# Optimization experiments

Hardware: AMD Instinct MI355X
Metric: run time of the kernel (lower is better)

The kernel has to match this reference:

```python
import jax, jax.numpy as jnp
import numpy as np

SEQ = 4096
EMBED = 1024


def setup_inputs() -> dict:
    key = jax.random.key(0)
    k1, k2 = jax.random.split(key)
    x = jax.random.normal(k1, (SEQ, EMBED), dtype=jnp.float32)
    # torch Linear(embed, 3*embed): store transposed weight so y = x @ W + b
    W = jax.random.normal(k2, (EMBED, 3 * EMBED), dtype=jnp.float32) * (1.0 / np.sqrt(EMBED))
    b = jnp.zeros((3 * EMBED,), dtype=jnp.float32)
    return {"x": x, "W": W, "b": b}


def reference(x, W, b):
    # QKV projection: [S, 3E] -> chunk along features
    qkv = x @ W + b
    q, k, v = jnp.split(qkv, 3, axis=1)  # each [S, E]
    d = q.shape[-1]
    scale = jnp.sqrt(jnp.asarray(d, dtype=x.dtype))
    logits = (q @ k.T) / scale  # [S, S]
    S = q.shape[0]
    causal = jnp.triu(jnp.ones((S, S), dtype=bool), k=1)
    logits = jnp.where(causal, -jnp.inf, logits)
    w = jax.nn.softmax(logits, axis=1)
    return w @ v  # [S, E]
```

## Files before the change

### kernel.cpp

```cpp
#include <hip/hip_runtime.h>

typedef short s16x8 __attribute__((ext_vector_type(8)));
typedef unsigned short u16;
typedef u16 u16x8 __attribute__((ext_vector_type(8)));
typedef float f32x4 __attribute__((ext_vector_type(4)));

#define SEQ 4096
#define EMBED 1024
#define NQKV 3072

static __device__ __forceinline__ u16 f2bf(float f) {
  unsigned int u = __float_as_uint(f);
  u += 0x7fffu + ((u >> 16) & 1u);
  return (u16)(u >> 16);
}
static __device__ __forceinline__ float bf2f(u16 b) {
  return __uint_as_float(((unsigned int)b) << 16);
}

static __device__ __forceinline__ f32x4 mfma16(s16x8 a, s16x8 b, f32x4 c) {
  return __builtin_amdgcn_mfma_f32_16x16x32_bf16(a, b, c, 0, 0, 0);
}

static __device__ __forceinline__ void gl2lds(const u16* g, u16* l) {
  __builtin_amdgcn_global_load_lds(
      (const __attribute__((address_space(1))) unsigned int*)g,
      (__attribute__((address_space(3))) unsigned int*)l, 16, 0, 0);
}

#define WAITVM(n) asm volatile("s_waitcnt vmcnt(" #n ")" ::: "memory")
#define LGKM0 asm volatile("s_waitcnt lgkmcnt(0)" ::: "memory")
#define BAR() asm volatile("s_waitcnt lgkmcnt(0)\n\ts_barrier" ::: "memory")

__global__ __launch_bounds__(256) void conv_x(const float* __restrict__ x,
                                              u16* __restrict__ xbf) {
  const size_t base = ((size_t)blockIdx.x * 256 + threadIdx.x) * 16;
  u16 tmp[16];
#pragma unroll
  for (int p = 0; p < 4; ++p) {
    float4 v = *reinterpret_cast<const float4*>(&x[base + p * 4]);
    tmp[p * 4 + 0] = f2bf(v.x); tmp[p * 4 + 1] = f2bf(v.y);
    tmp[p * 4 + 2] = f2bf(v.z); tmp[p * 4 + 3] = f2bf(v.w);
  }
  *reinterpret_cast<u16x8*>(&xbf[base]) = *reinterpret_cast<u16x8*>(&tmp[0]);
  *reinterpret_cast<u16x8*>(&xbf[base + 8]) = *reinterpret_cast<u16x8*>(&tmp[8]);
}

__global__ __launch_bounds__(256) void conv_wT(const float* __restrict__ W,
                                               u16* __restrict__ wT) {
  __shared__ u16 t[64][72];
  const int n0 = blockIdx.x * 64;
  const int k0 = blockIdx.y * 64;
  const int tid = threadIdx.x;
  const int rr = tid >> 3, c8 = (tid & 7) * 8;
#pragma unroll
  for (int p = 0; p < 2; ++p) {
    int r = p * 32 + rr;
    float4 a = *reinterpret_cast<const float4*>(&W[(size_t)(k0 + r) * NQKV + n0 + c8]);
    float4 b = *reinterpret_cast<const float4*>(&W[(size_t)(k0 + r) * NQKV + n0 + c8 + 4]);
    t[r][c8 + 0] = f2bf(a.x); t[r][c8 + 1] = f2bf(a.y);
    t[r][c8 + 2] = f2bf(a.z); t[r][c8 + 3] = f2bf(a.w);
    t[r][c8 + 4] = f2bf(b.x); t[r][c8 + 5] = f2bf(b.y);
    t[r][c8 + 6] = f2bf(b.z); t[r][c8 + 7] = f2bf(b.w);
  }
  __syncthreads();
#pragma unroll
  for (int p = 0; p < 2; ++p) {
    int c = p * 32 + rr;
    u16x8 v;
#pragma unroll
    for (int j = 0; j < 8; ++j) v[j] = t[c8 + j][c];
    *reinterpret_cast<u16x8*>(&wT[(size_t)(n0 + c) * EMBED + k0 + c8]) = v;
  }
}


#define GSTAGE32(dst_off, srcbase, stride)                                    \
  {                                                                           \
    _Pragma("unroll") for (int p_ = 0; p_ < 2; ++p_) {                        \
      gl2lds((srcbase) + (size_t)(p_ * 64 + w * 16 + (l >> 2)) * (stride) +   \
                 (l & 3) * 8,                                                 \
             lds_ + (dst_off) + p_ * 2048 + w * 512);                         \
    }                                                                         \
  }

#define MFMA_STEP(aoff, boff)                                                 \
  {                                                                           \
    s16x8 af[4], bfr[4];                                                      \
    _Pragma("unroll") for (int mb = 0; mb < 4; ++mb)                          \
        af[mb] = *reinterpret_cast<const s16x8*>(                             \
            &lds_[(aoff) + (wr + mb * 16 + lr) * 32 + lg * 8]);               \
    _Pragma("unroll") for (int nb = 0; nb < 4; ++nb)                          \
        bfr[nb] = *reinterpret_cast<const s16x8*>(                            \
            &lds_[(boff) + (wc + nb * 16 + lr) * 32 + lg * 8]);               \
    _Pragma("unroll") for (int mb = 0; mb < 4; ++mb)                          \
        _Pragma("unroll") for (int nb = 0; nb < 4; ++nb)                      \
            acc[mb][nb] = mfma16(af[mb], bfr[nb], acc[mb][nb]);               \
  }

#define KLOOP2(n, SRC_A, SA_STRIDE, SRC_B, SB_STRIDE)                         \
  GSTAGE32(0, SRC_A(0), SA_STRIDE);                                           \
  GSTAGE32(8192, SRC_B(0), SB_STRIDE);                                        \
  for (int t = 0; t < (n); ++t) {                                             \
    const int cur_ = t & 1, nx_ = cur_ ^ 1;                                   \
    if (t + 1 < (n)) {                                                        \
      LGKM0;                                                                  \
      GSTAGE32(nx_ * 4096, SRC_A(t + 1), SA_STRIDE);                          \
      GSTAGE32(8192 + nx_ * 4096, SRC_B(t + 1), SB_STRIDE);                   \
      WAITVM(4);                                                              \
    } else {                                                                  \
      WAITVM(0);                                                              \
    }                                                                         \
    BAR();                                                                    \
    MFMA_STEP(cur_ * 4096, 8192 + cur_ * 4096);                               \
    BAR();                                                                    \
  }

__global__ __launch_bounds__(256) void qkv_gemm(const u16* __restrict__ xbf,
                                                const u16* __restrict__ wT,
                                                const float* __restrict__ bias,
                                                u16* __restrict__ qkv,
                                                u16* __restrict__ vT) {
  __shared__ u16 lds_[17408];
  const int b = blockIdx.x;
  const int bs = (b & 7) * 96 + (b >> 3);
  const int bm = bs / 24, bn = bs % 24;
  const int m0 = bm * 128, n0 = bn * 128;
  const int tid = threadIdx.x;
  const int w = tid >> 6, l = tid & 63;
  const int wr = (w >> 1) * 64, wc = (w & 1) * 64;
  const int lg = l >> 4, lr = l & 15;

  f32x4 acc[4][4];
#pragma unroll
  for (int i = 0; i < 4; ++i)
#pragma unroll
    for (int j = 0; j < 4; ++j) acc[i][j] = (f32x4){0.f, 0.f, 0.f, 0.f};

  const u16* xa = xbf + (size_t)m0 * EMBED;
  const u16* wb = wT + (size_t)n0 * EMBED;
#define QA_SRC(t) (xa + (t) * 32)
#define QB_SRC(t) (wb + (t) * 32)
  KLOOP2(32, QA_SRC, EMBED, QB_SRC, EMBED);
#undef QA_SRC
#undef QB_SRC

  if (n0 < 2 * EMBED) {
#pragma unroll
    for (int mb = 0; mb < 4; ++mb)
#pragma unroll
      for (int nb = 0; nb < 4; ++nb) {
        const int col = n0 + wc + nb * 16 + lr;
        const float bv = bias[col];
#pragma unroll
        for (int e = 0; e < 4; ++e) {
          const int row = m0 + wr + mb * 16 + lg * 4 + e;
          qkv[(size_t)row * NQKV + col] = f2bf(acc[mb][nb][e] + bv);
        }
      }
  } else {
    const int vb = n0 - 2 * EMBED;
    __syncthreads();
#pragma unroll
    for (int mb = 0; mb < 4; ++mb)
#pragma unroll
      for (int nb = 0; nb < 4; ++nb) {
        const int cc = wc + nb * 16 + lr;
        const float bv = bias[n0 + cc];
#pragma unroll
        for (int e = 0; e < 4; ++e)
          lds_[(wr + mb * 16 + lg * 4 + e) * 136 + cc] = f2bf(acc[mb][nb][e] + bv);
      }
    __syncthreads();
    const int c = tid >> 1, hf = tid & 1;
#pragma unroll
    for (int j = 0; j < 8; ++j) {
      u16x8 v;
#pragma unroll
      for (int e2 = 0; e2 < 8; ++e2) v[e2] = lds_[(hf * 64 + j * 8 + e2) * 136 + c];
      *reinterpret_cast<u16x8*>(&vT[(size_t)(vb + c) * SEQ + m0 + hf * 64 + j * 8]) = v;
    }
  }
}

__global__ __launch_bounds__(256) void s_gemm(const u16* __restrict__ qkv,
                                              u16* __restrict__ Sp) {
  __shared__ u16 lds_[16384];
  const int b = blockIdx.x;
  const int bs = (b & 7) * 66 + (b >> 3);
  int mt = 0, cum = 0;
  while (cum + mt + 1 <= bs) { cum += mt + 1; ++mt; }
  const int nt = bs - cum;
  const int m0 = mt * 128, n0 = nt * 128;
  const int tid = threadIdx.x;
  const int w = tid >> 6, l = tid & 63;
  const int wr = (w >> 1) * 64, wc = (w & 1) * 64;
  const int lg = l >> 4, lr = l & 15;

  f32x4 acc[4][4];
#pragma unroll
  for (int i = 0; i < 4; ++i)
#pragma unroll
    for (int j = 0; j < 4; ++j) acc[i][j] = (f32x4){0.f, 0.f, 0.f, 0.f};

  const u16* qa = qkv + (size_t)m0 * NQKV;
  const u16* kb = qkv + (size_t)n0 * NQKV + EMBED;
#define SA_SRC(t) (qa + (t) * 32)
#define SB_SRC(t) (kb + (t) * 32)
  KLOOP2(32, SA_SRC, NQKV, SB_SRC, NQKV);
#undef SA_SRC
#undef SB_SRC

  u16* base = Sp + (size_t)bs * 16384;
#pragma unroll
  for (int mb = 0; mb < 4; ++mb)
#pragma unroll
    for (int nb = 0; nb < 4; ++nb) {
      const int cn = wc + nb * 16 + lr;
#pragma unroll
      for (int e = 0; e < 4; ++e) {
        const int rm = wr + mb * 16 + lg * 4 + e;
        base[rm * 128 + cn] = f2bf(acc[mb][nb][e] * 0.03125f);
      }
    }
}

__global__ __launch_bounds__(256) void softmax_rows(u16* __restrict__ Sp) {
  __shared__ float red[8];
  const int bid = blockIdx.x;
  const int tid = threadIdx.x;
  const int w = tid >> 6, l = tid & 63;
  const float NEG = -3.0e38f;

  for (int half = 0; half < 2; ++half) {
    const int r = half ? (4095 - bid) : bid;
    const int mt = r >> 7, rr = r & 127;
    const int Lp = (mt + 1) << 7;
    const size_t tri = (size_t)mt * (mt + 1) / 2;

    float v[16];
    float mx = NEG;
#pragma unroll
    for (int s = 0; s < 2; ++s) {
      const int j = tid * 8 + s * 2048;
      if (j < Lp) {
        const u16* p = Sp + (tri + (j >> 7)) * 16384 + rr * 128 + (j & 127);
        u16x8 xv = *reinterpret_cast<const u16x8*>(p);
#pragma unroll
        for (int e = 0; e < 8; ++e) {
          float f = (j + e <= r) ? bf2f(xv[e]) : NEG;
          v[s * 8 + e] = f;
          mx = fmaxf(mx, f);
        }
      } else {
#pragma unroll
        for (int e = 0; e < 8; ++e) v[s * 8 + e] = NEG;
      }
    }
#pragma unroll
    for (int off = 32; off >= 1; off >>= 1) mx = fmaxf(mx, __shfl_xor(mx, off, 64));
    if (l == 0) red[w] = mx;
    __syncthreads();
    mx = fmaxf(fmaxf(red[0], red[1]), fmaxf(red[2], red[3]));

    float sum = 0.f;
#pragma unroll
    for (int i = 0; i < 16; ++i) {
      float e = __expf(v[i] - mx);
      v[i] = e;
      sum += e;
    }
#pragma unroll
    for (int off = 32; off >= 1; off >>= 1) sum += __shfl_xor(sum, off, 64);
    if (l == 0) red[4 + w] = sum;
    __syncthreads();
    sum = red[4] + red[5] + red[6] + red[7];
    const float inv = 1.f / sum;

#pragma unroll
    for (int s = 0; s < 2; ++s) {
      const int j = tid * 8 + s * 2048;
      if (j < Lp) {
        u16x8 pk;
#pragma unroll
        for (int e = 0; e < 8; ++e) pk[e] = f2bf(v[s * 8 + e] * inv);
        *reinterpret_cast<u16x8*>(Sp + (tri + (j >> 7)) * 16384 + rr * 128 + (j & 127)) = pk;
      }
    }
    __syncthreads();
  }
}

__global__ __launch_bounds__(256) void pv_gemm(const u16* __restrict__ Sp,
                                               const u16* __restrict__ vT,
                                               float* __restrict__ out) {
  __shared__ u16 lds_[16384];
  const int nt = blockIdx.y;
  int s81 = blockIdx.x;
  int mt = 0, cum = 0, ls = 0;
  for (;;) {
    const int ns = (mt + 8) >> 3;
    if (s81 < cum + ns) { ls = s81 - cum; break; }
    cum += ns; ++mt;
  }
  const int m0 = mt * 128, n0 = nt * 128;
  const int k0 = ls * 1024;
  const int kext = (mt + 1) * 128;
  const int kend = (k0 + 1024 < kext) ? (k0 + 1024) : kext;
  const int ksteps = (kend - k0) >> 5;
  const size_t tri = (size_t)mt * (mt + 1) / 2;

  const int tid = threadIdx.x;
  const int w = tid >> 6, l = tid & 63;
  const int wr = (w >> 1) * 64, wc = (w & 1) * 64;
  const int lg = l >> 4, lr = l & 15;

  f32x4 acc[4][4];
#pragma unroll
  for (int i = 0; i < 4; ++i)
#pragma unroll
    for (int j = 0; j < 4; ++j) acc[i][j] = (f32x4){0.f, 0.f, 0.f, 0.f};

#define PA_SRC(t) (Sp + (tri + ((k0 + (t)*32) >> 7)) * 16384 + ((k0 + (t)*32) & 127))
#define PB_SRC(t) (vT + (size_t)n0 * SEQ + k0 + (t)*32)
  KLOOP2(ksteps, PA_SRC, 128, PB_SRC, SEQ);
#undef PA_SRC
#undef PB_SRC

#pragma unroll
  for (int mb = 0; mb < 4; ++mb)
#pragma unroll
    for (int nb = 0; nb < 4; ++nb) {
      const int col = n0 + wc + nb * 16 + lr;
#pragma unroll
      for (int e = 0; e < 4; ++e) {
        const int row = m0 + wr + mb * 16 + lg * 4 + e;
        unsafeAtomicAdd(&out[(size_t)row * EMBED + col], acc[mb][nb][e]);
      }
    }
}

__global__ __launch_bounds__(512) void attn_fb(const u16* __restrict__ qkv,
                                               const u16* __restrict__ vT,
                                               float* __restrict__ out) {
  __shared__ u16 q_lds[16][1032];
  __shared__ u16 kv_lds[8][3][2048];
  __shared__ u16 p_lds[16][136];
  __shared__ float redmax[8][16];
  __shared__ float redsum[8][16];
  const int bid = blockIdx.x;
  const int tid = threadIdx.x;
  const int w = tid >> 6, l = tid & 63;
  const int lg = l >> 4, lr = l & 15;

  const int sr = l >> 4;
  const int scb = (l & 15) * 16;
  const int scolA = ((scb ^ (sr << 4)) >> 1);
  const int scolB = ((scb ^ ((4 + sr) << 4)) >> 1);
  int boff[4];
#pragma unroll
  for (int kk = 0; kk < 4; ++kk)
    boff[kk] = lr * 256 + ((kk * 64 + lg * 16) ^ ((lr & 7) << 4));

  u16* kvb[3] = {&kv_lds[w][0][0], &kv_lds[w][1][0], &kv_lds[w][2][0]};

#define STAGE_K(dc, bufp)                                                     \
  {                                                                           \
    LGKM0;                                                                    \
    const u16* g0 = qkv + (size_t)(kb + w * 16 + sr) * NQKV + EMBED + (dc) * 128; \
    gl2lds(g0 + scolA, (bufp));                                               \
    gl2lds(g0 + 4 * NQKV + scolB, (bufp) + 512);                              \
    gl2lds(g0 + 8 * NQKV + scolA, (bufp) + 1024);                             \
    gl2lds(g0 + 12 * NQKV + scolB, (bufp) + 1536);                            \
  }
#define STAGE_V(j, bufp)                                                      \
  {                                                                           \
    LGKM0;                                                                    \
    const u16* g0 = vT + (size_t)((j) * 128 + w * 16 + sr) * SEQ + kb;        \
    gl2lds(g0 + scolA, (bufp));                                               \
    gl2lds(g0 + 4 * SEQ + scolB, (bufp) + 512);                               \
    gl2lds(g0 + 8 * SEQ + scolA, (bufp) + 1024);                              \
    gl2lds(g0 + 12 * SEQ + scolB, (bufp) + 1536);                             \
  }

  const int qb = bid * 16;
  __syncthreads();
#pragma unroll
  for (int p = 0; p < 4; ++p) {
    int idx = p * 512 + tid;
    int r = idx >> 7, c = (idx & 127) * 8;
    *reinterpret_cast<u16x8*>(&q_lds[r][c]) =
        *reinterpret_cast<const u16x8*>(&qkv[(size_t)(qb + r) * NQKV + c]);
  }
  __syncthreads();
  s16x8 qf[32];
#pragma unroll
  for (int kk = 0; kk < 32; ++kk)
    qf[kk] = *reinterpret_cast<const s16x8*>(&q_lds[lr][kk * 32 + lg * 8]);

  f32x4 o_acc[8];
#pragma unroll
  for (int j = 0; j < 8; ++j) o_acc[j] = (f32x4){0.f, 0.f, 0.f, 0.f};
  float m_st[4], l_st[4];
#pragma unroll
  for (int e = 0; e < 4; ++e) { m_st[e] = -__builtin_inff(); l_st[e] = 0.f; }

  const int n_it = (qb >> 7) + 1;
  for (int it = 0; it < n_it; ++it) {
    const int kb = it << 7;
    const int kcol = kb + w * 16 + lr;

    f32x4 s = (f32x4){0.f, 0.f, 0.f, 0.f};
    STAGE_K(0, kvb[0]);
    STAGE_K(1, kvb[1]);
#pragma unroll
    for (int dc = 0; dc < 8; ++dc) {
      if (dc < 6) {
        STAGE_K(dc + 2, kvb[(dc + 2) % 3]);
      } else if (dc == 6) {
        STAGE_V(0, kvb[2]);
      } else {
        STAGE_V(1, kvb[0]);
      }
      WAITVM(8);
      u16* cur = kvb[dc % 3];
#pragma unroll
      for (int kk = 0; kk < 4; ++kk) {
        s16x8 bfr = *reinterpret_cast<const s16x8*>((const char*)cur + boff[kk]);
        s = mfma16(qf[dc * 4 + kk], bfr, s);
      }
    }

    float sv[4], mx[4];
#pragma unroll
    for (int e = 0; e < 4; ++e) {
      float v = s[e] * 0.03125f;
      sv[e] = (kcol > qb + lg * 4 + e) ? -__builtin_inff() : v;
      mx[e] = sv[e];
    }
#pragma unroll
    for (int off = 1; off < 16; off <<= 1)
#pragma unroll
      for (int e = 0; e < 4; ++e) mx[e] = fmaxf(mx[e], __shfl_xor(mx[e], off, 64));
    if (lr == 0) {
#pragma unroll
      for (int e = 0; e < 4; ++e) redmax[w][lg * 4 + e] = mx[e];
    }
    BAR();

    float m_new[4], sc[4], pv[4], rs[4];
#pragma unroll
    for (int e = 0; e < 4; ++e) {
      float m = m_st[e];
#pragma unroll
      for (int ww = 0; ww < 8; ++ww) m = fmaxf(m, redmax[ww][lg * 4 + e]);
      m_new[e] = m;
      sc[e] = __expf(m_st[e] - m);
      pv[e] = __expf(sv[e] - m);
      rs[e] = pv[e];
    }
#pragma unroll
    for (int off = 1; off < 16; off <<= 1)
#pragma unroll
      for (int e = 0; e < 4; ++e) rs[e] += __shfl_xor(rs[e], off, 64);
    if (lr == 0) {
#pragma unroll
      for (int e = 0; e < 4; ++e) redsum[w][lg * 4 + e] = rs[e];
    }
#pragma unroll
    for (int e = 0; e < 4; ++e) p_lds[lg * 4 + e][w * 16 + lr] = f2bf(pv[e]);
    BAR();

#pragma unroll
    for (int e = 0; e < 4; ++e) {
      float a2 = l_st[e] * sc[e];
#pragma unroll
      for (int ww = 0; ww < 8; ++ww) a2 += redsum[ww][lg * 4 + e];
      l_st[e] = a2;
      m_st[e] = m_new[e];
    }
#pragma unroll
    for (int j = 0; j < 8; ++j)
#pragma unroll
      for (int e = 0; e < 4; ++e) o_acc[j][e] *= sc[e];

    s16x8 pa[4];
#pragma unroll
    for (int kk = 0; kk < 4; ++kk)
      pa[kk] = *reinterpret_cast<const s16x8*>(&p_lds[lr][kk * 32 + lg * 8]);

#pragma unroll
    for (int j = 0; j < 8; ++j) {
      if (j < 6) {
        STAGE_V(j + 2, kvb[(j + 4) % 3]);
        WAITVM(8);
      } else if (j == 6) {
        WAITVM(4);
      } else {
        WAITVM(0);
      }
      u16* cur = kvb[(j + 2) % 3];
#pragma unroll
      for (int kk = 0; kk < 4; ++kk) {
        s16x8 bfr = *reinterpret_cast<const s16x8*>((const char*)cur + boff[kk]);
        o_acc[j] = mfma16(pa[kk], bfr, o_acc[j]);
      }
    }
  }

#pragma unroll
  for (int j = 0; j < 8; ++j) {
    const int col = j * 128 + w * 16 + lr;
#pragma unroll
    for (int e = 0; e < 4; ++e)
      out[(size_t)(qb + lg * 4 + e) * EMBED + col] = o_acc[j][e] / l_st[e];
  }
#undef STAGE_K
#undef STAGE_V
}

extern "C" void kernel_launch(void* const* d_in, const int* in_sizes, int n_in,
                              void* d_out, int out_size, void* d_ws, size_t ws_size,
                              hipStream_t stream) {
  (void)in_sizes; (void)n_in; (void)out_size;
  const float* x = (const float*)d_in[0];
  const float* W = (const float*)d_in[1];
  const float* bias = (const float*)d_in[2];
  float* out = (float*)d_out;

  u16* qkv = (u16*)d_ws;
  u16* vT = qkv + (size_t)SEQ * NQKV;
  u16* wT = (u16*)d_out;
  u16* Sp = (u16*)((char*)d_ws + (32u << 20));

  const size_t need = (32u << 20) + (size_t)528 * 16384 * 2;
  const bool big = ws_size >= need;
  u16* xbf = big ? Sp : (u16*)((char*)d_out + (8u << 20));

  conv_x<<<(SEQ * EMBED) / (256 * 16), 256, 0, stream>>>(x, xbf);
  conv_wT<<<dim3(NQKV / 64, EMBED / 64), 256, 0, stream>>>(W, wT);
  qkv_gemm<<<(SEQ / 128) * (NQKV / 128), 256, 0, stream>>>(xbf, wT, bias, qkv, vT);

  if (big) {
    s_gemm<<<528, 256, 0, stream>>>(qkv, Sp);
    softmax_rows<<<2048, 256, 0, stream>>>(Sp);
    hipMemsetAsync(d_out, 0, (size_t)SEQ * EMBED * sizeof(float), stream);
    pv_gemm<<<dim3(80, 8), 256, 0, stream>>>(Sp, vT, out);
  } else {
    attn_fb<<<SEQ / 16, 512, 0, stream>>>(qkv, vT, out);
  }
}
```

Baseline: 150.1 us.

## Enlarge GEMM tiles to 256x128 across qkv, score and PV kernels

Each workgroup now computes a 256x128 output tile, with 8x4 MFMA accumulators per wave, instead of 128x128. This applies to all three GEMM kernels and is meant to raise operand reuse and cut global/LDS traffic per flop. The causal triangle tiling is remapped so that S blocks skip upper tiles at store time. PV uses a zeroed scratch buffer for the out-of-triangle half of the A tile. In exchange it uses more registers and LDS, launches fewer blocks, wastes some compute on masked tiles, and adds a memset.

```diff
diff --git a/kernel.cpp b/kernel.cpp
--- a/kernel.cpp
+++ b/kernel.cpp
@@ -75,7 +75,7 @@
 }
 
 
-#define GSTAGE32(dst_off, srcbase, stride)                                    \
+#define GST2(dst_off, srcbase, stride)                                        \
   {                                                                           \
     _Pragma("unroll") for (int p_ = 0; p_ < 2; ++p_) {                        \
       gl2lds((srcbase) + (size_t)(p_ * 64 + w * 16 + (l >> 2)) * (stride) +   \
@@ -84,145 +84,160 @@
     }                                                                         \
   }
 
-#define MFMA_STEP(aoff, boff)                                                 \
+#define MFMA256(aoff, boff)                                                   \
   {                                                                           \
-    s16x8 af[4], bfr[4];                                                      \
-    _Pragma("unroll") for (int mb = 0; mb < 4; ++mb)                          \
-        af[mb] = *reinterpret_cast<const s16x8*>(                             \
-            &lds_[(aoff) + (wr + mb * 16 + lr) * 32 + lg * 8]);               \
+    s16x8 af[8], bfr[4];                                                      \
+    _Pragma("unroll") for (int mi = 0; mi < 8; ++mi)                          \
+        af[mi] = *reinterpret_cast<const s16x8*>(                             \
+            &lds_[(aoff) + (wm * 128 + mi * 16 + lr) * 32 + lg * 8]);         \
     _Pragma("unroll") for (int nb = 0; nb < 4; ++nb)                          \
         bfr[nb] = *reinterpret_cast<const s16x8*>(                            \
-            &lds_[(boff) + (wc + nb * 16 + lr) * 32 + lg * 8]);               \
-    _Pragma("unroll") for (int mb = 0; mb < 4; ++mb)                          \
+            &lds_[(boff) + (wn * 64 + nb * 16 + lr) * 32 + lg * 8]);          \
+    _Pragma("unroll") for (int mi = 0; mi < 8; ++mi)                          \
         _Pragma("unroll") for (int nb = 0; nb < 4; ++nb)                      \
-            acc[mb][nb] = mfma16(af[mb], bfr[nb], acc[mb][nb]);               \
-  }
-
-#define KLOOP2(n, SRC_A, SA_STRIDE, SRC_B, SB_STRIDE)                         \
-  GSTAGE32(0, SRC_A(0), SA_STRIDE);                                           \
-  GSTAGE32(8192, SRC_B(0), SB_STRIDE);                                        \
+            acc[mi][nb] = mfma16(af[mi], bfr[nb], acc[mi][nb]);               \
+  }
+
+#define KLOOP256(n, SRC_A0, SA0_STRIDE, SRC_A1, SA1_STRIDE, SRC_B, SB_STRIDE) \
+  GST2(0, SRC_A0(0), SA0_STRIDE);                                             \
+  GST2(4096, SRC_A1(0), SA1_STRIDE);                                          \
+  GST2(16384, SRC_B(0), SB_STRIDE);                                           \
   for (int t = 0; t < (n); ++t) {                                             \
     const int cur_ = t & 1, nx_ = cur_ ^ 1;                                   \
     if (t + 1 < (n)) {                                                        \
       LGKM0;                                                                  \
-      GSTAGE32(nx_ * 4096, SRC_A(t + 1), SA_STRIDE);                          \
-      GSTAGE32(8192 + nx_ * 4096, SRC_B(t + 1), SB_STRIDE);                   \
-      WAITVM(4);                                                              \
+      GST2(nx_ * 8192, SRC_A0(t + 1), SA0_STRIDE);                            \
+      GST2(nx_ * 8192 + 4096, SRC_A1(t + 1), SA1_STRIDE);                     \
+      GST2(16384 + nx_ * 4096, SRC_B(t + 1), SB_STRIDE);                      \
+      WAITVM(6);                                                              \
     } else {                                                                  \
       WAITVM(0);                                                              \
     }                                                                         \
     BAR();                                                                    \
-    MFMA_STEP(cur_ * 4096, 8192 + cur_ * 4096);                               \
+    MFMA256(cur_ * 8192, 16384 + cur_ * 4096);                                \
     BAR();                                                                    \
   }
+
+#define ACC_INIT                                                              \
+  f32x4 acc[8][4];                                                            \
+  _Pragma("unroll") for (int i_ = 0; i_ < 8; ++i_)                            \
+  _Pragma("unroll") for (int j_ = 0; j_ < 4; ++j_)                            \
+      acc[i_][j_] = (f32x4){0.f, 0.f, 0.f, 0.f};
 
 __global__ __launch_bounds__(256) void qkv_gemm(const u16* __restrict__ xbf,
                                                 const u16* __restrict__ wT,
                                                 const float* __restrict__ bias,
                                                 u16* __restrict__ qkv,
                                                 u16* __restrict__ vT) {
-  __shared__ u16 lds_[17408];
+  __shared__ u16 lds_[24576];
   const int b = blockIdx.x;
-  const int bs = (b & 7) * 96 + (b >> 3);
+  const int bs = (b & 7) * 48 + (b >> 3);
   const int bm = bs / 24, bn = bs % 24;
-  const int m0 = bm * 128, n0 = bn * 128;
+  const int m0 = bm * 256, n0 = bn * 128;
   const int tid = threadIdx.x;
   const int w = tid >> 6, l = tid & 63;
-  const int wr = (w >> 1) * 64, wc = (w & 1) * 64;
+  const int wm = w >> 1, wn = w & 1;
   const int lg = l >> 4, lr = l & 15;
 
-  f32x4 acc[4][4];
-#pragma unroll
-  for (int i = 0; i < 4; ++i)
-#pragma unroll
-    for (int j = 0; j < 4; ++j) acc[i][j] = (f32x4){0.f, 0.f, 0.f, 0.f};
-
-  const u16* xa = xbf + (size_t)m0 * EMBED;
+  ACC_INIT;
+
+  const u16* xa0 = xbf + (size_t)m0 * EMBED;
+  const u16* xa1 = xa0 + (size_t)128 * EMBED;
   const u16* wb = wT + (size_t)n0 * EMBED;
-#define QA_SRC(t) (xa + (t) * 32)
-#define QB_SRC(t) (wb + (t) * 32)
-  KLOOP2(32, QA_SRC, EMBED, QB_SRC, EMBED);
-#undef QA_SRC
-#undef QB_SRC
+#define QA0(t) (xa0 + (t) * 32)
+#define QA1(t) (xa1 + (t) * 32)
+#define QB(t) (wb + (t) * 32)
+  KLOOP256(32, QA0, EMBED, QA1, EMBED, QB, EMBED);
+#undef QA0
+#undef QA1
+#undef QB
 
   if (n0 < 2 * EMBED) {
 #pragma unroll
-    for (int mb = 0; mb < 4; ++mb)
+    for (int mi = 0; mi < 8; ++mi)
 #pragma unroll
       for (int nb = 0; nb < 4; ++nb) {
-        const int col = n0 + wc + nb * 16 + lr;
+        const int col = n0 + wn * 64 + nb * 16 + lr;
         const float bv = bias[col];
 #pragma unroll
         for (int e = 0; e < 4; ++e) {
-          const int row = m0 + wr + mb * 16 + lg * 4 + e;
-          qkv[(size_t)row * NQKV + col] = f2bf(acc[mb][nb][e] + bv);
+          const int row = m0 + wm * 128 + mi * 16 + lg * 4 + e;
+          qkv[(size_t)row * NQKV + col] = f2bf(acc[mi][nb][e] + bv);
         }
       }
   } else {
     const int vb = n0 - 2 * EMBED;
-    __syncthreads();
-#pragma unroll
-    for (int mb = 0; mb < 4; ++mb)
-#pragma unroll
-      for (int nb = 0; nb < 4; ++nb) {
-        const int cc = wc + nb * 16 + lr;
-        const float bv = bias[n0 + cc];
-#pragma unroll
-        for (int e = 0; e < 4; ++e)
-          lds_[(wr + mb * 16 + lg * 4 + e) * 136 + cc] = f2bf(acc[mb][nb][e] + bv);
-      }
-    __syncthreads();
-    const int c = tid >> 1, hf = tid & 1;
-#pragma unroll
-    for (int j = 0; j < 8; ++j) {
-      u16x8 v;
-#pragma unroll
-      for (int e2 = 0; e2 < 8; ++e2) v[e2] = lds_[(hf * 64 + j * 8 + e2) * 136 + c];
-      *reinterpret_cast<u16x8*>(&vT[(size_t)(vb + c) * SEQ + m0 + hf * 64 + j * 8]) = v;
+#pragma unroll
+    for (int h = 0; h < 2; ++h) {
+      __syncthreads();
+      if (wm == h) {
+#pragma unroll
+        for (int mi = 0; mi < 8; ++mi)
+#pragma unroll
+          for (int nb = 0; nb < 4; ++nb) {
+            const int cc = wn * 64 + nb * 16 + lr;
+            const float bv = bias[n0 + cc];
+#pragma unroll
+            for (int e = 0; e < 4; ++e)
+              lds_[(mi * 16 + lg * 4 + e) * 136 + cc] = f2bf(acc[mi][nb][e] + bv);
+          }
+      }
+      __syncthreads();
+      const int c = tid >> 1, hf = tid & 1;
+#pragma unroll
+      for (int j = 0; j < 8; ++j) {
+        u16x8 v;
+#pragma unroll
+        for (int e2 = 0; e2 < 8; ++e2) v[e2] = lds_[(hf * 64 + j * 8 + e2) * 136 + c];
+        *reinterpret_cast<u16x8*>(
+            &vT[(size_t)(vb + c) * SEQ + m0 + h * 128 + hf * 64 + j * 8]) = v;
+      }
     }
   }
 }
 
 __global__ __launch_bounds__(256) void s_gemm(const u16* __restrict__ qkv,
                                               u16* __restrict__ Sp) {
-  __shared__ u16 lds_[16384];
+  __shared__ u16 lds_[24576];
   const int b = blockIdx.x;
-  const int bs = (b & 7) * 66 + (b >> 3);
-  int mt = 0, cum = 0;
-  while (cum + mt + 1 <= bs) { cum += mt + 1; ++mt; }
-  const int nt = bs - cum;
-  const int m0 = mt * 128, n0 = nt * 128;
+  const int bs = (b & 7) * 34 + (b >> 3);
+  int mt = 0;
+  while ((mt + 1) * (mt + 2) <= bs) ++mt;
+  const int nt = bs - mt * (mt + 1);
+  const int m0 = mt * 256, n0 = nt * 128;
   const int tid = threadIdx.x;
   const int w = tid >> 6, l = tid & 63;
-  const int wr = (w >> 1) * 64, wc = (w & 1) * 64;
+  const int wm = w >> 1, wn = w & 1;
   const int lg = l >> 4, lr = l & 15;
 
-  f32x4 acc[4][4];
-#pragma unroll
-  for (int i = 0; i < 4; ++i)
-#pragma unroll
-    for (int j = 0; j < 4; ++j) acc[i][j] = (f32x4){0.f, 0.f, 0.f, 0.f};
-
-  const u16* qa = qkv + (size_t)m0 * NQKV;
+  ACC_INIT;
+
+  const u16* qa0 = qkv + (size_t)m0 * NQKV;
+  const u16* qa1 = qa0 + (size_t)128 * NQKV;
   const u16* kb = qkv + (size_t)n0 * NQKV + EMBED;
-#define SA_SRC(t) (qa + (t) * 32)
-#define SB_SRC(t) (kb + (t) * 32)
-  KLOOP2(32, SA_SRC, NQKV, SB_SRC, NQKV);
-#undef SA_SRC
-#undef SB_SRC
-
-  u16* base = Sp + (size_t)bs * 16384;
-#pragma unroll
-  for (int mb = 0; mb < 4; ++mb)
-#pragma unroll
-    for (int nb = 0; nb < 4; ++nb) {
-      const int cn = wc + nb * 16 + lr;
-#pragma unroll
-      for (int e = 0; e < 4; ++e) {
-        const int rm = wr + mb * 16 + lg * 4 + e;
-        base[rm * 128 + cn] = f2bf(acc[mb][nb][e] * 0.03125f);
-      }
-    }
+#define SA0(t) (qa0 + (t) * 32)
+#define SA1(t) (qa1 + (t) * 32)
+#define SB(t) (kb + (t) * 32)
+  KLOOP256(32, SA0, NQKV, SA1, NQKV, SB, NQKV);
+#undef SA0
+#undef SA1
+#undef SB
+
+  const int rb = 2 * mt + wm;
+  if (nt <= rb) {
+    u16* base = Sp + ((size_t)rb * (rb + 1) / 2 + nt) * 16384;
+#pragma unroll
+    for (int mi = 0; mi < 8; ++mi)
+#pragma unroll
+      for (int nb = 0; nb < 4; ++nb) {
+        const int cn = wn * 64 + nb * 16 + lr;
+#pragma unroll
+        for (int e = 0; e < 4; ++e) {
+          const int rm = mi * 16 + lg * 4 + e;
+          base[rm * 128 + cn] = f2bf(acc[mi][nb][e] * 0.03125f);
+        }
+      }
+  }
 }
 
 __global__ __launch_bounds__(256) void softmax_rows(u16* __restrict__ Sp) {
@@ -293,49 +308,53 @@
 
 __global__ __launch_bounds__(256) void pv_gemm(const u16* __restrict__ Sp,
                                                const u16* __restrict__ vT,
+                                               const u16* __restrict__ zp,
                                                float* __restrict__ out) {
-  __shared__ u16 lds_[16384];
+  __shared__ u16 lds_[24576];
   const int nt = blockIdx.y;
-  int s81 = blockIdx.x;
+  int sx = blockIdx.x;
   int mt = 0, cum = 0, ls = 0;
   for (;;) {
-    const int ns = (mt + 8) >> 3;
-    if (s81 < cum + ns) { ls = s81 - cum; break; }
+    const int ns = (2 * mt + 9) >> 3;
+    if (sx < cum + ns) { ls = sx - cum; break; }
     cum += ns; ++mt;
   }
-  const int m0 = mt * 128, n0 = nt * 128;
+  const int m0 = mt * 256, n0 = nt * 128;
   const int k0 = ls * 1024;
-  const int kext = (mt + 1) * 128;
+  const int kext = (2 * mt + 2) * 128;
   const int kend = (k0 + 1024 < kext) ? (k0 + 1024) : kext;
   const int ksteps = (kend - k0) >> 5;
-  const size_t tri = (size_t)mt * (mt + 1) / 2;
+  const size_t tri0 = (size_t)mt * (2 * mt + 1);
+  const size_t tri1 = (size_t)(2 * mt + 1) * (mt + 1);
 
   const int tid = threadIdx.x;
   const int w = tid >> 6, l = tid & 63;
-  const int wr = (w >> 1) * 64, wc = (w & 1) * 64;
+  const int wm = w >> 1, wn = w & 1;
   const int lg = l >> 4, lr = l & 15;
 
-  f32x4 acc[4][4];
-#pragma unroll
-  for (int i = 0; i < 4; ++i)
-#pragma unroll
-    for (int j = 0; j < 4; ++j) acc[i][j] = (f32x4){0.f, 0.f, 0.f, 0.f};
-
-#define PA_SRC(t) (Sp + (tri + ((k0 + (t)*32) >> 7)) * 16384 + ((k0 + (t)*32) & 127))
-#define PB_SRC(t) (vT + (size_t)n0 * SEQ + k0 + (t)*32)
-  KLOOP2(ksteps, PA_SRC, 128, PB_SRC, SEQ);
-#undef PA_SRC
-#undef PB_SRC
-
-#pragma unroll
-  for (int mb = 0; mb < 4; ++mb)
+  ACC_INIT;
+
+#define PKB(t) ((k0 + (t)*32) >> 7)
+#define PKC(t) ((k0 + (t)*32) & 127)
+#define PA0(t) ((PKB(t) <= 2 * mt) ? (Sp + (tri0 + PKB(t)) * 16384 + PKC(t)) : zp)
+#define PA1(t) (Sp + (tri1 + PKB(t)) * 16384 + PKC(t))
+#define PB(t) (vT + (size_t)n0 * SEQ + k0 + (t)*32)
+  KLOOP256(ksteps, PA0, 128, PA1, 128, PB, SEQ);
+#undef PA0
+#undef PA1
+#undef PB
+#undef PKB
+#undef PKC
+
+#pragma unroll
+  for (int mi = 0; mi < 8; ++mi)
 #pragma unroll
     for (int nb = 0; nb < 4; ++nb) {
-      const int col = n0 + wc + nb * 16 + lr;
+      const int col = n0 + wn * 64 + nb * 16 + lr;
 #pragma unroll
       for (int e = 0; e < 4; ++e) {
-        const int row = m0 + wr + mb * 16 + lg * 4 + e;
-        unsafeAtomicAdd(&out[(size_t)row * EMBED + col], acc[mb][nb][e]);
+        const int row = m0 + wm * 128 + mi * 16 + lg * 4 + e;
+        unsafeAtomicAdd(&out[(size_t)row * EMBED + col], acc[mi][nb][e]);
       }
     }
 }
@@ -532,20 +551,22 @@
   u16* vT = qkv + (size_t)SEQ * NQKV;
   u16* wT = (u16*)d_out;
   u16* Sp = (u16*)((char*)d_ws + (32u << 20));
-
-  const size_t need = (32u << 20) + (size_t)528 * 16384 * 2;
+  u16* zp = Sp + (size_t)528 * 16384;
+
+  const size_t need = (32u << 20) + (size_t)528 * 16384 * 2 + 32768;
   const bool big = ws_size >= need;
   u16* xbf = big ? Sp : (u16*)((char*)d_out + (8u << 20));
 
   conv_x<<<(SEQ * EMBED) / (256 * 16), 256, 0, stream>>>(x, xbf);
   conv_wT<<<dim3(NQKV / 64, EMBED / 64), 256, 0, stream>>>(W, wT);
-  qkv_gemm<<<(SEQ / 128) * (NQKV / 128), 256, 0, stream>>>(xbf, wT, bias, qkv, vT);
+  qkv_gemm<<<384, 256, 0, stream>>>(xbf, wT, bias, qkv, vT);
 
   if (big) {
-    s_gemm<<<528, 256, 0, stream>>>(qkv, Sp);
+    hipMemsetAsync(zp, 0, 32768, stream);
+    s_gemm<<<272, 256, 0, stream>>>(qkv, Sp);
     softmax_rows<<<2048, 256, 0, stream>>>(Sp);
     hipMemsetAsync(d_out, 0, (size_t)SEQ * EMBED * sizeof(float), stream);
-    pv_gemm<<<dim3(80, 8), 256, 0, stream>>>(Sp, vT, out);
+    pv_gemm<<<dim3(40, 8), 256, 0, stream>>>(Sp, vT, zp, out);
   } else {
     attn_fb<<<SEQ / 16, 512, 0, stream>>>(qkv, vT, out);
   }
```

New measurement: 203.8 us. 1.36x slower.

## Fuse conversion kernels, reorder pv_gemm blocks, use plain stores for single-split rows

Applied to the files above, without the earlier changes.

Merges the x and W bf16 conversion kernels into one launch with a branched block index. In pv_gemm, the block-to-tile mapping is reordered so the first 52 blocks take the full 1024-wide K splits and the rest take the tail splits. Row tiles with a single K split (mt<=7) now write output with plain stores instead of atomics, so the memset shrinks to skip the first 1024 rows. This trims a launch, part of the memset traffic and some atomic contention, at the cost of more complex index logic.

```diff
diff --git a/kernel.cpp b/kernel.cpp
--- a/kernel.cpp
+++ b/kernel.cpp
@@ -32,45 +32,47 @@
 #define LGKM0 asm volatile("s_waitcnt lgkmcnt(0)" ::: "memory")
 #define BAR() asm volatile("s_waitcnt lgkmcnt(0)\n\ts_barrier" ::: "memory")
 
-__global__ __launch_bounds__(256) void conv_x(const float* __restrict__ x,
-                                              u16* __restrict__ xbf) {
-  const size_t base = ((size_t)blockIdx.x * 256 + threadIdx.x) * 16;
-  u16 tmp[16];
-#pragma unroll
-  for (int p = 0; p < 4; ++p) {
-    float4 v = *reinterpret_cast<const float4*>(&x[base + p * 4]);
-    tmp[p * 4 + 0] = f2bf(v.x); tmp[p * 4 + 1] = f2bf(v.y);
-    tmp[p * 4 + 2] = f2bf(v.z); tmp[p * 4 + 3] = f2bf(v.w);
-  }
-  *reinterpret_cast<u16x8*>(&xbf[base]) = *reinterpret_cast<u16x8*>(&tmp[0]);
-  *reinterpret_cast<u16x8*>(&xbf[base + 8]) = *reinterpret_cast<u16x8*>(&tmp[8]);
-}
-
-__global__ __launch_bounds__(256) void conv_wT(const float* __restrict__ W,
-                                               u16* __restrict__ wT) {
+__global__ __launch_bounds__(256) void conv_fused(const float* __restrict__ x,
+                                                  const float* __restrict__ W,
+                                                  u16* __restrict__ xbf,
+                                                  u16* __restrict__ wT) {
   __shared__ u16 t[64][72];
-  const int n0 = blockIdx.x * 64;
-  const int k0 = blockIdx.y * 64;
   const int tid = threadIdx.x;
-  const int rr = tid >> 3, c8 = (tid & 7) * 8;
-#pragma unroll
-  for (int p = 0; p < 2; ++p) {
-    int r = p * 32 + rr;
-    float4 a = *reinterpret_cast<const float4*>(&W[(size_t)(k0 + r) * NQKV + n0 + c8]);
-    float4 b = *reinterpret_cast<const float4*>(&W[(size_t)(k0 + r) * NQKV + n0 + c8 + 4]);
-    t[r][c8 + 0] = f2bf(a.x); t[r][c8 + 1] = f2bf(a.y);
-    t[r][c8 + 2] = f2bf(a.z); t[r][c8 + 3] = f2bf(a.w);
-    t[r][c8 + 4] = f2bf(b.x); t[r][c8 + 5] = f2bf(b.y);
-    t[r][c8 + 6] = f2bf(b.z); t[r][c8 + 7] = f2bf(b.w);
-  }
-  __syncthreads();
-#pragma unroll
-  for (int p = 0; p < 2; ++p) {
-    int c = p * 32 + rr;
-    u16x8 v;
-#pragma unroll
-    for (int j = 0; j < 8; ++j) v[j] = t[c8 + j][c];
-    *reinterpret_cast<u16x8*>(&wT[(size_t)(n0 + c) * EMBED + k0 + c8]) = v;
+  if (blockIdx.x < 1024) {
+    const size_t base = ((size_t)blockIdx.x * 256 + tid) * 16;
+    u16 tmp[16];
+#pragma unroll
+    for (int p = 0; p < 4; ++p) {
+      float4 v = *reinterpret_cast<const float4*>(&x[base + p * 4]);
+      tmp[p * 4 + 0] = f2bf(v.x); tmp[p * 4 + 1] = f2bf(v.y);
+      tmp[p * 4 + 2] = f2bf(v.z); tmp[p * 4 + 3] = f2bf(v.w);
+    }
+    *reinterpret_cast<u16x8*>(&xbf[base]) = *reinterpret_cast<u16x8*>(&tmp[0]);
+    *reinterpret_cast<u16x8*>(&xbf[base + 8]) = *reinterpret_cast<u16x8*>(&tmp[8]);
+  } else {
+    const int b2 = blockIdx.x - 1024;
+    const int n0 = (b2 % 48) * 64;
+    const int k0 = (b2 / 48) * 64;
+    const int rr = tid >> 3, c8 = (tid & 7) * 8;
+#pragma unroll
+    for (int p = 0; p < 2; ++p) {
+      int r = p * 32 + rr;
+      float4 a = *reinterpret_cast<const float4*>(&W[(size_t)(k0 + r) * NQKV + n0 + c8]);
+      float4 b = *reinterpret_cast<const float4*>(&W[(size_t)(k0 + r) * NQKV + n0 + c8 + 4]);
+      t[r][c8 + 0] = f2bf(a.x); t[r][c8 + 1] = f2bf(a.y);
+      t[r][c8 + 2] = f2bf(a.z); t[r][c8 + 3] = f2bf(a.w);
+      t[r][c8 + 4] = f2bf(b.x); t[r][c8 + 5] = f2bf(b.y);
+      t[r][c8 + 6] = f2bf(b.z); t[r][c8 + 7] = f2bf(b.w);
+    }
+    __syncthreads();
+#pragma unroll
+    for (int p = 0; p < 2; ++p) {
+      int c = p * 32 + rr;
+      u16x8 v;
+#pragma unroll
+      for (int j = 0; j < 8; ++j) v[j] = t[c8 + j][c];
+      *reinterpret_cast<u16x8*>(&wT[(size_t)(n0 + c) * EMBED + k0 + c8]) = v;
+    }
   }
 }
 
@@ -296,12 +298,25 @@
                                                float* __restrict__ out) {
   __shared__ u16 lds_[16384];
   const int nt = blockIdx.y;
-  int s81 = blockIdx.x;
-  int mt = 0, cum = 0, ls = 0;
-  for (;;) {
-    const int ns = (mt + 8) >> 3;
-    if (s81 < cum + ns) { ls = s81 - cum; break; }
-    cum += ns; ++mt;
+  const int sx = blockIdx.x;
+  int mt, ls;
+  if (sx < 52) {
+    int m = 0, c = 0;
+    for (;;) {
+      const int f = (m + 1) >> 3;
+      if (sx < c + f) { ls = sx - c; break; }
+      c += f; ++m;
+    }
+    mt = m;
+  } else {
+    const int r = sx - 52;
+    int m = 0, c = 0;
+    for (;;) {
+      if (((m + 1) & 7) != 0) { if (c == r) break; ++c; }
+      ++m;
+    }
+    mt = m;
+    ls = (mt + 1) >> 3;
   }
   const int m0 = mt * 128, n0 = nt * 128;
   const int k0 = ls * 1024;
@@ -327,17 +342,31 @@
 #undef PA_SRC
 #undef PB_SRC
 
-#pragma unroll
-  for (int mb = 0; mb < 4; ++mb)
-#pragma unroll
-    for (int nb = 0; nb < 4; ++nb) {
-      const int col = n0 + wc + nb * 16 + lr;
-#pragma unroll
-      for (int e = 0; e < 4; ++e) {
-        const int row = m0 + wr + mb * 16 + lg * 4 + e;
-        unsafeAtomicAdd(&out[(size_t)row * EMBED + col], acc[mb][nb][e]);
-      }
-    }
+  if (mt <= 7) {
+#pragma unroll
+    for (int mb = 0; mb < 4; ++mb)
+#pragma unroll
+      for (int nb = 0; nb < 4; ++nb) {
+        const int col = n0 + wc + nb * 16 + lr;
+#pragma unroll
+        for (int e = 0; e < 4; ++e) {
+          const int row = m0 + wr + mb * 16 + lg * 4 + e;
+          out[(size_t)row * EMBED + col] = acc[mb][nb][e];
+        }
+      }
+  } else {
+#pragma unroll
+    for (int mb = 0; mb < 4; ++mb)
+#pragma unroll
+      for (int nb = 0; nb < 4; ++nb) {
+        const int col = n0 + wc + nb * 16 + lr;
+#pragma unroll
+        for (int e = 0; e < 4; ++e) {
+          const int row = m0 + wr + mb * 16 + lg * 4 + e;
+          unsafeAtomicAdd(&out[(size_t)row * EMBED + col], acc[mb][nb][e]);
+        }
+      }
+  }
 }
 
 __global__ __launch_bounds__(512) void attn_fb(const u16* __restrict__ qkv,
@@ -537,14 +566,14 @@
   const bool big = ws_size >= need;
   u16* xbf = big ? Sp : (u16*)((char*)d_out + (8u << 20));
 
-  conv_x<<<(SEQ * EMBED) / (256 * 16), 256, 0, stream>>>(x, xbf);
-  conv_wT<<<dim3(NQKV / 64, EMBED / 64), 256, 0, stream>>>(W, wT);
+  conv_fused<<<1792, 256, 0, stream>>>(x, W, xbf, (u16*)d_out);
   qkv_gemm<<<(SEQ / 128) * (NQKV / 128), 256, 0, stream>>>(xbf, wT, bias, qkv, vT);
 
   if (big) {
     s_gemm<<<528, 256, 0, stream>>>(qkv, Sp);
     softmax_rows<<<2048, 256, 0, stream>>>(Sp);
-    hipMemsetAsync(d_out, 0, (size_t)SEQ * EMBED * sizeof(float), stream);
+    hipMemsetAsync((char*)d_out + (size_t)1024 * EMBED * sizeof(float), 0,
+                   (size_t)(SEQ - 1024) * EMBED * sizeof(float), stream);
     pv_gemm<<<dim3(80, 8), 256, 0, stream>>>(Sp, vT, out);
   } else {
     attn_fb<<<SEQ / 16, 512, 0, stream>>>(qkv, vT, out);
```

Result: faster. 146.1 us (-2.7%).
